# Performance work log

Hardware: AMD Instinct MI355X
Metric: run time of the kernel (lower is better)

Reference implementation:

```python
import jax, jax.numpy as jnp
import numpy as np
from jax import lax


def _conv(x, w):
    # 3x3 conv, stride 1, SAME padding, NCHW/OIHW layout, no bias
    return lax.conv_general_dilated(
        x, w, window_strides=(1, 1), padding='SAME',
        dimension_numbers=('NCHW', 'OIHW', 'NCHW'))


def _interleave2x2(tl, tr, bl, br):
    # each [B,H,W] -> [B,2H,2W] with tl at (0::2,0::2), tr at (0::2,1::2), etc.
    top = jnp.stack([tl, tr], axis=-1)          # [B,H,W,2]
    bot = jnp.stack([bl, br], axis=-1)          # [B,H,W,2]
    x = jnp.stack([top, bot], axis=2)           # [B,H,2,W,2]
    B, H, _, W, _ = x.shape
    return x.reshape(B, 2 * H, 2 * W)


def setup_inputs() -> dict:
    key = jax.random.key(0)
    ks = jax.random.split(key, 8)
    B, H, W = 16, 512, 512
    width = 12
    s = 0.1  # weight scale, approximates xavier for tiny fan-ins
    return {
        'mosaic': jax.random.normal(ks[0], (B, 4, H, W), jnp.float32),
        'fw0': jax.random.normal(ks[1], (width, 4, 3, 3), jnp.float32) * s,
        'fw1': jax.random.normal(ks[2], (width, width, 3, 3), jnp.float32) * s,
        'fw2': jax.random.normal(ks[3], (width, width, 3, 3), jnp.float32) * s,
        'ww0': jax.random.normal(ks[4], (width, 4, 3, 3), jnp.float32) * s,
        'ww1': jax.random.normal(ks[5], (width, width, 3, 3), jnp.float32) * s,
        'ww2': jax.random.normal(ks[6], (width, width, 3, 3), jnp.float32) * s,
        'cw0': jax.random.normal(ks[7], (6, 2, 3, 3), jnp.float32) * s,
    }


def reference(mosaic, fw0, fw1, fw2, ww0, ww1, ww2, cw0):
    width = fw0.shape[0]  # 12
    half = width // 2

    f = jax.nn.relu(_conv(mosaic, fw0))
    f = jax.nn.relu(_conv(f, fw1))
    interps = jax.nn.relu(_conv(f, fw2))

    w = jax.nn.relu(_conv(mosaic, ww0))
    w = jax.nn.relu(_conv(w, ww1))
    w = jax.nn.relu(_conv(w, ww2))
    weights = jax.nn.softmax(w, axis=1)

    mul = interps * weights                              # [B,12,H,W]
    # green_rb[:,0] = sum of first half, green_rb[:,1] = sum of second half
    green_rb = jnp.stack(
        [mul[:, :half].sum(axis=1), mul[:, half:].sum(axis=1)], axis=1)  # [B,2,H,W]

    # green_add channels: [mosaic0, g1, mosaic3, mosaic0, g0, mosaic3]
    green_add = jnp.stack([
        mosaic[:, 0], green_rb[:, 1], mosaic[:, 3],
        mosaic[:, 0], green_rb[:, 0], mosaic[:, 3]], axis=1)  # [B,6,H,W]

    # chroma: (rb - green_rb) -> single conv 2->6 (chroma_depth=1, no relu)
    rb = jnp.stack([mosaic[:, 1], mosaic[:, 2]], axis=1)  # [B,2,H,W]
    chroma_diff = _conv(rb - green_rb, cw0)               # [B,6,H,W]
    chroma_pred = chroma_diff + green_add

    # pixel-shuffle assembly of full-res RGB [B,3,2H,2W]
    r = _interleave2x2(chroma_pred[:, 0], mosaic[:, 1], chroma_pred[:, 1], chroma_pred[:, 2])
    g = _interleave2x2(mosaic[:, 0], green_rb[:, 0], green_rb[:, 1], mosaic[:, 3])
    b = _interleave2x2(chroma_pred[:, 3], chroma_pred[:, 4], mosaic[:, 2], chroma_pred[:, 5])
    return jnp.stack([r, g, b], axis=1)
```

## Files before the change

### kernel.cpp

```cpp
#include <hip/hip_runtime.h>
#include <cstdint>

#define HH 512
#define WW 512
#define TX 58

typedef __attribute__((ext_vector_type(8)))  short    short8;
typedef __attribute__((ext_vector_type(16))) float    f32x16;
typedef __attribute__((ext_vector_type(4)))  float    f32x4;
typedef __attribute__((ext_vector_type(2)))  unsigned u32x2;
typedef __attribute__((ext_vector_type(8)))  int      int8v;

union FragU { uint4 u; short8 s; };
union B8U   { u32x2 u2[2]; short8 s; };
union AF8   { uint4 u[2]; int8v v; };
union BF8   { unsigned d[8]; int8v v; };

#define L1F_O  0
#define L1W_O  9984
#define L1RST  832
#define MOS_O  19968
#define MOSR   512
#define L2F_O  19968
#define L2W_O  28288
#define L2RST  832
#define RELAY_O 0
#define SMEMB  36608

#define MFMA_SC(A, B, C) \
  __builtin_amdgcn_mfma_scale_f32_16x16x128_f8f6f4((A), (B), (C), 0, 0, 0, 0x7F7F7F7Fu, 0, 0x7F7F7F7Fu)

__device__ __forceinline__ unsigned cvtpk(float a, float b) {
  unsigned r;
  asm("v_cvt_pk_bf16_f32 %0, %1, %2" : "=v"(r) : "v"(a), "v"(b));
  return r;
}
__device__ __forceinline__ unsigned rpk8(float a, float b, float c, float d, bool im) {
  int r = __builtin_amdgcn_cvt_pk_fp8_f32(fmaxf(a, 0.f), fmaxf(b, 0.f), 0, false);
  r = __builtin_amdgcn_cvt_pk_fp8_f32(fmaxf(c, 0.f), fmaxf(d, 0.f), r, true);
  return im ? (unsigned)r : 0u;
}
__device__ __forceinline__ unsigned short f2bf(float f) {
  union { float f; unsigned u; } v; v.f = f;
  unsigned r = v.u + 0x7fffu + ((v.u >> 16) & 1u);
  return (unsigned short)(r >> 16);
}
__device__ __forceinline__ float bf2f(unsigned short b) {
  union { unsigned u; float f; } v; v.u = ((unsigned)b) << 16;
  return v.f;
}
__device__ __forceinline__ float lo16(unsigned u) {
  union { unsigned v; float f; } x; x.v = u << 16; return x.f;
}
__device__ __forceinline__ float hi16(unsigned u) {
  union { unsigned v; float f; } x; x.v = u & 0xffff0000u; return x.f;
}

__global__ void wt_kernel(const float* __restrict__ fw0, const float* __restrict__ fw1,
                          const float* __restrict__ fw2, const float* __restrict__ ww0,
                          const float* __restrict__ ww1, const float* __restrict__ ww2,
                          uint4* __restrict__ wsf) {
  int t = blockIdx.x * 256 + threadIdx.x;
  if (t >= 448) return;
  if (t < 192) {
    int f = t >> 6, lane = t & 63;
    int h = (lane >> 5) & 1, m = lane & 31;
    unsigned short v[8];
#pragma unroll
    for (int e = 0; e < 8; ++e) {
      int sq = 2 * h + (e >> 2);
      int c4 = e & 3;
      float w = 0.f;
      if (sq < 3 && m < 24) {
        w = (m < 12) ? fw0[(m * 4 + c4) * 9 + f * 3 + sq]
                     : ww0[((m - 12) * 4 + c4) * 9 + f * 3 + sq];
      }
      v[e] = f2bf(w);
    }
    uint4 o;
    o.x = (unsigned)v[0] | ((unsigned)v[1] << 16);
    o.y = (unsigned)v[2] | ((unsigned)v[3] << 16);
    o.z = (unsigned)v[4] | ((unsigned)v[5] << 16);
    o.w = (unsigned)v[6] | ((unsigned)v[7] << 16);
    wsf[t] = o;
  } else {
    int u = t - 192, sid = u >> 6, lane = u & 63;
    int m = lane & 15, kg = lane >> 4;
    int layer = sid >> 1, path = sid & 1;
    const float* src = layer ? (path ? ww2 : fw2) : (path ? ww1 : fw1);
    const float scale = (layer == 1 && path == 1) ? 1.44269504f : 1.0f;
    unsigned d[8];
#pragma unroll
    for (int k = 0; k < 8; ++k) {
      float w4[4];
#pragma unroll
      for (int j4 = 0; j4 < 4; ++j4) {
        int e = 4 * k + j4;
        float w = 0.f;
        if (m < 12) {
          if (kg < 3) {
            int dx = e / 12, ci = e % 12, tap = kg * 3 + dx;
            w = src[(m * 12 + ci) * 9 + tap] * scale;
          } else {
            int i = e >> 3, j = e & 7;
            if (i < 3 && j < 4) {
              int tap = i * 3 + 2, ci = 8 + j;
              w = src[(m * 12 + ci) * 9 + tap] * scale;
            }
          }
        }
        w4[j4] = w;
      }
      int x = __builtin_amdgcn_cvt_pk_fp8_f32(w4[0], w4[1], 0, false);
      x = __builtin_amdgcn_cvt_pk_fp8_f32(w4[2], w4[3], x, true);
      d[k] = (unsigned)x;
    }
    uint4* dst = wsf + 192 + sid * 128 + lane * 2;
    dst[0] = make_uint4(d[0], d[1], d[2], d[3]);
    dst[1] = make_uint4(d[4], d[5], d[6], d[7]);
  }
}

__global__ __launch_bounds__(256, 4)
void green_kernel(const float* __restrict__ mosaic, const uint4* __restrict__ wsf,
                  unsigned short* __restrict__ green) {
  __shared__ __align__(16) char s[SMEMB];
  const int tid = threadIdx.x;
  const int lane = tid & 63;
  const int wv = __builtin_amdgcn_readfirstlane(tid >> 6);
  const int h = (lane >> 5) & 1, ln = lane & 31;
  const int ln8 = ln * 8, ln12 = ln * 12;
  const int pxl = lane & 15, kg = lane >> 4;
  const int bid = blockIdx.x;
  const int bx = bid % 9;
  const int t9 = bid / 9;
  const int by = t9 & 63, b = t9 >> 6;
  const int X0 = bx * TX, Y0 = by * 8;

  {
    const float* mb = mosaic + (size_t)b * 4 * HH * WW;
    for (int p = tid; p < 14 * 64; p += 256) {
      int row = p >> 6, col = p & 63;
      int gy = Y0 + row - 3, gx = X0 + col - 3;
      float c0 = 0.f, c1 = 0.f, c2 = 0.f, c3 = 0.f;
      if ((unsigned)gy < HH && (unsigned)gx < WW) {
        const float* mp = mb + (size_t)gy * WW + gx;
        c0 = mp[0]; c1 = mp[HH * WW]; c2 = mp[2 * HH * WW]; c3 = mp[3 * HH * WW];
      }
      u32x2 w = { cvtpk(c0, c1), cvtpk(c2, c3) };
      *(u32x2*)(s + MOS_O + row * MOSR + col * 8) = w;
    }
    for (int i = tid; i < 528; i += 256) {
      int seg = i / 22, d = i - seg * 22;
      int row = seg % 12, w = seg / 12;
      *(unsigned*)(s + w * 9984 + row * 832 + 744 + d * 4) = 0u;
    }
  }
  __syncthreads();

  {
    FragU a3[3];
#pragma unroll
    for (int q = 0; q < 3; ++q) a3[q].u = wsf[q * 64 + lane];
    const char* pLo = s + MOS_O + 3 * wv * MOSR + ln8 + 16 * h;
    const char* pHi = s + MOS_O + 3 * wv * MOSR + ln8 + 8;
    char* base = s + 3 * wv * L1RST + ln12;
    char* pA = base + L1F_O + 4 * h;
    char* pB = h ? base + L1W_O : base + L1F_O + 8;
    char* pC = base + L1W_O + (h ? 8 : 4);
    bool ck[2];
    ck[0] = (unsigned)(X0 + 0  + ln - 2) < WW;
    ck[1] = (unsigned)(X0 + 30 + ln - 2) < WW;
#pragma unroll
    for (int r = 0; r < 3; ++r) {
      const int ly = 3 * wv + r;
      const bool rowok = (unsigned)(Y0 + ly - 2) < HH;
#pragma unroll
      for (int g = 0; g < 2; ++g) {
        const int cb = g * 30;
        f32x16 c = {};
#pragma unroll
        for (int ky = 0; ky < 3; ++ky) {
          B8U bu;
          bu.u2[0] = *(const u32x2*)(pLo + (r + ky) * MOSR + cb * 8);
          bu.u2[1] = *(const u32x2*)(pHi + (r + ky) * MOSR + cb * 8);
          c = __builtin_amdgcn_mfma_f32_32x32x16_bf16(a3[ky].s, bu.s, c, 0, 0, 0);
        }
        const bool im = rowok && ck[g];
        *(unsigned*)(pA + r * L1RST + cb * 12) = rpk8(c[0], c[1], c[2], c[3], im);
        *(unsigned*)(pB + r * L1RST + cb * 12) = rpk8(c[4], c[5], c[6], c[7], im);
        *(unsigned*)(pC + r * L1RST + cb * 12) = rpk8(c[8], c[9], c[10], c[11], im);
      }
    }
  }
  __syncthreads();

  {
    for (int i = tid; i < 560; i += 256) {
      int seg = i / 28, d = i - seg * 28;
      int row = seg % 10, w = seg / 10;
      *(unsigned*)(s + L2F_O + w * 8320 + row * 832 + 720 + d * 4) = 0u;
    }
    AF8 aF, aW;
    aF.u[0] = wsf[192 + lane * 2]; aF.u[1] = wsf[193 + lane * 2];
    aW.u[0] = wsf[320 + lane * 2]; aW.u[1] = wsf[321 + lane * 2];
    const int c0 = (wv == 0) ? 0 : (wv == 1) ? 16 : (wv == 2) ? 32 : 44;
    int o0, o1, o2, o3;
    if (kg < 3) { o0 = kg * L1RST + pxl * 12; o1 = o0 + 8; o2 = o0 + 16; o3 = o0 + 24; }
    else        { o0 = (pxl + 2) * 12 + 8; o1 = o0 + L1RST; o2 = o1 + L1RST; o3 = o2; }
    const char* P0 = s + L1F_O + c0 * 12 + o0;
    const char* P1 = s + L1F_O + c0 * 12 + o1;
    const char* P2 = s + L1F_O + c0 * 12 + o2;
    const char* P3 = s + L1F_O + c0 * 12 + o3;
    const bool ckx = (unsigned)(X0 + c0 + pxl - 1) < WW;
    char* pO = s + L2F_O + (c0 + pxl) * 12 + 4 * kg;
#pragma unroll
    for (int ly = 0; ly < 10; ++ly) {
      const int imm = ly * L1RST;
      BF8 bF, bW;
      bF.d[0] = *(const unsigned*)(P0 + imm);        bF.d[1] = *(const unsigned*)(P0 + imm + 4);
      bF.d[2] = *(const unsigned*)(P1 + imm);        bF.d[3] = *(const unsigned*)(P1 + imm + 4);
      bF.d[4] = *(const unsigned*)(P2 + imm);        bF.d[5] = *(const unsigned*)(P2 + imm + 4);
      bF.d[6] = *(const unsigned*)(P3 + imm);        bF.d[7] = *(const unsigned*)(P3 + imm + 4);
      bW.d[0] = *(const unsigned*)(P0 + imm + 9984); bW.d[1] = *(const unsigned*)(P0 + imm + 9988);
      bW.d[2] = *(const unsigned*)(P1 + imm + 9984); bW.d[3] = *(const unsigned*)(P1 + imm + 9988);
      bW.d[4] = *(const unsigned*)(P2 + imm + 9984); bW.d[5] = *(const unsigned*)(P2 + imm + 9988);
      bW.d[6] = *(const unsigned*)(P3 + imm + 9984); bW.d[7] = *(const unsigned*)(P3 + imm + 9988);
      f32x4 cF = {0.f, 0.f, 0.f, 0.f}, cW = {0.f, 0.f, 0.f, 0.f};
      cF = MFMA_SC(aF.v, bF.v, cF);
      cW = MFMA_SC(aW.v, bW.v, cW);
      const bool im = ckx && ((unsigned)(Y0 + ly - 1) < HH);
      if (kg < 3) {
        *(unsigned*)(pO + ly * L2RST)        = rpk8(cF[0], cF[1], cF[2], cF[3], im);
        *(unsigned*)(pO + ly * L2RST + 8320) = rpk8(cW[0], cW[1], cW[2], cW[3], im);
      }
    }
  }
  __syncthreads();

  {
    AF8 aF, aW;
    aF.u[0] = wsf[448 + lane * 2]; aF.u[1] = wsf[449 + lane * 2];
    aW.u[0] = wsf[576 + lane * 2]; aW.u[1] = wsf[577 + lane * 2];
    const int c0 = (wv == 0) ? 0 : (wv == 1) ? 16 : (wv == 2) ? 32 : 42;
    int o0, o1, o2, o3;
    if (kg < 3) { o0 = kg * L2RST + pxl * 12; o1 = o0 + 8; o2 = o0 + 16; o3 = o0 + 24; }
    else        { o0 = (pxl + 2) * 12 + 8; o1 = o0 + L2RST; o2 = o1 + L2RST; o3 = o2; }
    const char* P0 = s + L2F_O + c0 * 12 + o0;
    const char* P1 = s + L2F_O + c0 * 12 + o1;
    const char* P2 = s + L2F_O + c0 * 12 + o2;
    const char* P3 = s + L2F_O + c0 * 12 + o3;
    char* relay = s + RELAY_O + wv * 3328;
#pragma unroll
    for (int half = 0; half < 2; ++half) {
#pragma unroll
      for (int rr = 0; rr < 4; ++rr) {
        const int imm = (half * 4 + rr) * L2RST;
        BF8 bF, bW;
        bF.d[0] = *(const unsigned*)(P0 + imm);        bF.d[1] = *(const unsigned*)(P0 + imm + 4);
        bF.d[2] = *(const unsigned*)(P1 + imm);        bF.d[3] = *(const unsigned*)(P1 + imm + 4);
        bF.d[4] = *(const unsigned*)(P2 + imm);        bF.d[5] = *(const unsigned*)(P2 + imm + 4);
        bF.d[6] = *(const unsigned*)(P3 + imm);        bF.d[7] = *(const unsigned*)(P3 + imm + 4);
        bW.d[0] = *(const unsigned*)(P0 + imm + 8320); bW.d[1] = *(const unsigned*)(P0 + imm + 8324);
        bW.d[2] = *(const unsigned*)(P1 + imm + 8320); bW.d[3] = *(const unsigned*)(P1 + imm + 8324);
        bW.d[4] = *(const unsigned*)(P2 + imm + 8320); bW.d[5] = *(const unsigned*)(P2 + imm + 8324);
        bW.d[6] = *(const unsigned*)(P3 + imm + 8320); bW.d[7] = *(const unsigned*)(P3 + imm + 8324);
        f32x4 cF = {0.f, 0.f, 0.f, 0.f}, cW = {0.f, 0.f, 0.f, 0.f};
        cF = MFMA_SC(aF.v, bF.v, cF);
        cW = MFMA_SC(aW.v, bW.v, cW);
        if (kg < 3) {
          char* slot = relay + ((rr << 4) + pxl) * 52 + kg * 8;
          *(unsigned*)(slot)      = cvtpk(fmaxf(cF[0], 0.f), fmaxf(cF[1], 0.f));
          *(unsigned*)(slot + 4)  = cvtpk(fmaxf(cF[2], 0.f), fmaxf(cF[3], 0.f));
          *(unsigned*)(slot + 24) = cvtpk(fmaxf(cW[0], 0.f), fmaxf(cW[1], 0.f));
          *(unsigned*)(slot + 28) = cvtpk(fmaxf(cW[2], 0.f), fmaxf(cW[3], 0.f));
        }
      }
      asm volatile("s_waitcnt lgkmcnt(0)" ::: "memory");
      {
        const char* slot = relay + lane * 52;
        unsigned fu[6], wu[6];
#pragma unroll
        for (int i = 0; i < 6; ++i) {
          fu[i] = *(const unsigned*)(slot + i * 4);
          wu[i] = *(const unsigned*)(slot + 24 + i * 4);
        }
        float F[12], Wv[12];
#pragma unroll
        for (int i = 0; i < 6; ++i) {
          F[2 * i] = lo16(fu[i]);  F[2 * i + 1] = hi16(fu[i]);
          Wv[2 * i] = lo16(wu[i]); Wv[2 * i + 1] = hi16(wu[i]);
        }
        float m = 0.f;
#pragma unroll
        for (int c2 = 0; c2 < 12; ++c2) m = fmaxf(m, Wv[c2]);
        float sum = 0.f, s0 = 0.f, s1 = 0.f;
#pragma unroll
        for (int c2 = 0; c2 < 12; ++c2) {
          const float e = exp2f(Wv[c2] - m);
          sum += e;
          if (c2 < 6) s0 = fmaf(F[c2], e, s0);
          else        s1 = fmaf(F[c2], e, s1);
        }
        const float inv = 1.f / sum;
        const unsigned pg = cvtpk(s0 * inv, s1 * inv);
        const int gy = Y0 + half * 4 + kg;
        const int gx = X0 + c0 + pxl;
        if ((unsigned)gx < WW) {
          green[((b * 2 + 0) * HH + gy) * WW + gx] = (unsigned short)pg;
          green[((b * 2 + 1) * HH + gy) * WW + gx] = (unsigned short)(pg >> 16);
        }
      }
      asm volatile("s_waitcnt lgkmcnt(0)" ::: "memory");
    }
  }
}

__global__ __launch_bounds__(256)
void assemble_kernel(const float* __restrict__ mosaic, const unsigned short* __restrict__ green,
                     const float* __restrict__ cw0, float* __restrict__ out) {
  const int t = blockIdx.x * 256 + threadIdx.x;
  const int x = t & (WW - 1);
  const int y = (t >> 9) & (HH - 1);
  const int b = t >> 18;

  const int p = y * WW + x;
  const float* __restrict__ mb = mosaic + (size_t)b * 4 * HH * WW;
  const unsigned short* __restrict__ gb = green + (size_t)b * 2 * HH * WW;

  const float m0 = mb[p];
  const float m1 = mb[HH * WW + p];
  const float m2 = mb[2 * HH * WW + p];
  const float m3 = mb[3 * HH * WW + p];
  const float g0 = bf2f(gb[p]);
  const float g1 = bf2f(gb[HH * WW + p]);

  float cd[6] = {0.f, 0.f, 0.f, 0.f, 0.f, 0.f};
#pragma unroll
  for (int ky = 0; ky < 3; ++ky) {
#pragma unroll
    for (int kx = 0; kx < 3; ++kx) {
      const int yy = y + ky - 1, xx = x + kx - 1;
      float c0 = 0.f, c1 = 0.f;
      if ((unsigned)yy < HH && (unsigned)xx < WW) {
        const int q = yy * WW + xx;
        c0 = mb[HH * WW + q]     - bf2f(gb[q]);
        c1 = mb[2 * HH * WW + q] - bf2f(gb[HH * WW + q]);
      }
      const int k = ky * 3 + kx;
#pragma unroll
      for (int o = 0; o < 6; ++o) {
        cd[o] = fmaf(c0, cw0[(o * 2 + 0) * 9 + k], cd[o]);
        cd[o] = fmaf(c1, cw0[(o * 2 + 1) * 9 + k], cd[o]);
      }
    }
  }
  const float cp0 = cd[0] + m0;
  const float cp1 = cd[1] + g1;
  const float cp2 = cd[2] + m3;
  const float cp3 = cd[3] + m0;
  const float cp4 = cd[4] + g0;
  const float cp5 = cd[5] + m3;

  const int W2 = 2 * WW;
  const size_t plane = (size_t)(2 * HH) * W2;
  size_t base = ((size_t)(b * 3) * (2 * HH) + 2 * y) * W2 + 2 * x;
  *(float2*)(out + base)              = make_float2(cp0, m1);
  *(float2*)(out + base + W2)         = make_float2(cp1, cp2);
  *(float2*)(out + base + plane)      = make_float2(m0, g0);
  *(float2*)(out + base + plane + W2) = make_float2(g1, m3);
  *(float2*)(out + base + 2 * plane)      = make_float2(cp3, cp4);
  *(float2*)(out + base + 2 * plane + W2) = make_float2(m2, cp5);
}

extern "C" void kernel_launch(void* const* d_in, const int* in_sizes, int n_in,
                              void* d_out, int out_size, void* d_ws, size_t ws_size,
                              hipStream_t stream) {
  const float* mosaic = (const float*)d_in[0];
  const float* fw0 = (const float*)d_in[1];
  const float* fw1 = (const float*)d_in[2];
  const float* fw2 = (const float*)d_in[3];
  const float* ww0 = (const float*)d_in[4];
  const float* ww1 = (const float*)d_in[5];
  const float* ww2 = (const float*)d_in[6];
  const float* cw0 = (const float*)d_in[7];

  uint4* wsf = (uint4*)((char*)d_ws + 32768);
  unsigned short* green = (unsigned short*)((char*)d_ws + 67584);
  float* out = (float*)d_out;

  wt_kernel<<<2, 256, 0, stream>>>(fw0, fw1, fw2, ww0, ww1, ww2, wsf);
  green_kernel<<<16 * 64 * 9, 256, 0, stream>>>(mosaic, wsf, green);
  assemble_kernel<<<(16 * HH * WW) / 256, 256, 0, stream>>>(mosaic, green, cw0, out);
}
```

Before: 193.7 us.

## Fuse chroma conv and RGB assembly into green kernel via extra halo

Merges the separate assemble kernel into the green kernel. Each tile now computes green with one extra halo pixel on every side, stores it in LDS, then runs the 2->6 chroma conv and writes the interleaved RGB output directly. This removes the global write and re-read of the bf16 green planes and one kernel launch. In exchange it redoes more halo work per tile in the conv layers, uses more LDS, and lowers the occupancy bound from 4 to 3 blocks.

Measured after the change: 229.8 us. 1.19x slower.

```diff
diff --git a/kernel.cpp b/kernel.cpp
--- a/kernel.cpp
+++ b/kernel.cpp
@@ -17,15 +17,16 @@
 union BF8   { unsigned d[8]; int8v v; };
 
 #define L1F_O  0
-#define L1W_O  9984
+#define L1W_O  11648
 #define L1RST  832
-#define MOS_O  19968
-#define MOSR   512
-#define L2F_O  19968
-#define L2W_O  28288
+#define MOS_O  23296
+#define MOSR   528
+#define L2F_O  23296
+#define L2W_O  33280
 #define L2RST  832
 #define RELAY_O 0
-#define SMEMB  36608
+#define GLDS_O 13312
+#define SMEMB  43264
 
 #define MFMA_SC(A, B, C) \
   __builtin_amdgcn_mfma_scale_f32_16x16x128_f8f6f4((A), (B), (C), 0, 0, 0, 0x7F7F7F7Fu, 0, 0x7F7F7F7Fu)
@@ -44,10 +45,6 @@
   union { float f; unsigned u; } v; v.f = f;
   unsigned r = v.u + 0x7fffu + ((v.u >> 16) & 1u);
   return (unsigned short)(r >> 16);
-}
-__device__ __forceinline__ float bf2f(unsigned short b) {
-  union { unsigned u; float f; } v; v.u = ((unsigned)b) << 16;
-  return v.f;
 }
 __device__ __forceinline__ float lo16(unsigned u) {
   union { unsigned v; float f; } x; x.v = u << 16; return x.f;
@@ -121,9 +118,9 @@
   }
 }
 
-__global__ __launch_bounds__(256, 4)
+__global__ __launch_bounds__(256, 3)
 void green_kernel(const float* __restrict__ mosaic, const uint4* __restrict__ wsf,
-                  unsigned short* __restrict__ green) {
+                  const float* __restrict__ cw0, float* __restrict__ out) {
   __shared__ __align__(16) char s[SMEMB];
   const int tid = threadIdx.x;
   const int lane = tid & 63;
@@ -136,12 +133,12 @@
   const int t9 = bid / 9;
   const int by = t9 & 63, b = t9 >> 6;
   const int X0 = bx * TX, Y0 = by * 8;
+  const float* __restrict__ mb = mosaic + (size_t)b * 4 * HH * WW;
 
   {
-    const float* mb = mosaic + (size_t)b * 4 * HH * WW;
-    for (int p = tid; p < 14 * 64; p += 256) {
-      int row = p >> 6, col = p & 63;
-      int gy = Y0 + row - 3, gx = X0 + col - 3;
+    for (int p = tid; p < 16 * 66; p += 256) {
+      int row = p / 66, col = p - row * 66;
+      int gy = Y0 + row - 4, gx = X0 + col - 4;
       float c0 = 0.f, c1 = 0.f, c2 = 0.f, c3 = 0.f;
       if ((unsigned)gy < HH && (unsigned)gx < WW) {
         const float* mp = mb + (size_t)gy * WW + gx;
@@ -150,10 +147,10 @@
       u32x2 w = { cvtpk(c0, c1), cvtpk(c2, c3) };
       *(u32x2*)(s + MOS_O + row * MOSR + col * 8) = w;
     }
-    for (int i = tid; i < 528; i += 256) {
-      int seg = i / 22, d = i - seg * 22;
-      int row = seg % 12, w = seg / 12;
-      *(unsigned*)(s + w * 9984 + row * 832 + 744 + d * 4) = 0u;
+    for (int i = tid; i < 448; i += 256) {
+      int seg = i >> 4, d = i & 15;
+      int row = seg % 14, w = seg / 14;
+      *(unsigned*)(s + w * 11648 + row * 832 + 768 + d * 4) = 0u;
     }
   }
   __syncthreads();
@@ -162,49 +159,51 @@
     FragU a3[3];
 #pragma unroll
     for (int q = 0; q < 3; ++q) a3[q].u = wsf[q * 64 + lane];
-    const char* pLo = s + MOS_O + 3 * wv * MOSR + ln8 + 16 * h;
-    const char* pHi = s + MOS_O + 3 * wv * MOSR + ln8 + 8;
-    char* base = s + 3 * wv * L1RST + ln12;
+    const char* pLo = s + MOS_O + 4 * wv * MOSR + ln8 + 16 * h;
+    const char* pHi = s + MOS_O + 4 * wv * MOSR + ln8 + 8;
+    char* base = s + 4 * wv * L1RST + ln12;
     char* pA = base + L1F_O + 4 * h;
     char* pB = h ? base + L1W_O : base + L1F_O + 8;
     char* pC = base + L1W_O + (h ? 8 : 4);
     bool ck[2];
-    ck[0] = (unsigned)(X0 + 0  + ln - 2) < WW;
-    ck[1] = (unsigned)(X0 + 30 + ln - 2) < WW;
-#pragma unroll
-    for (int r = 0; r < 3; ++r) {
-      const int ly = 3 * wv + r;
-      const bool rowok = (unsigned)(Y0 + ly - 2) < HH;
-#pragma unroll
-      for (int g = 0; g < 2; ++g) {
-        const int cb = g * 30;
-        f32x16 c = {};
-#pragma unroll
-        for (int ky = 0; ky < 3; ++ky) {
-          B8U bu;
-          bu.u2[0] = *(const u32x2*)(pLo + (r + ky) * MOSR + cb * 8);
-          bu.u2[1] = *(const u32x2*)(pHi + (r + ky) * MOSR + cb * 8);
-          c = __builtin_amdgcn_mfma_f32_32x32x16_bf16(a3[ky].s, bu.s, c, 0, 0, 0);
-        }
-        const bool im = rowok && ck[g];
-        *(unsigned*)(pA + r * L1RST + cb * 12) = rpk8(c[0], c[1], c[2], c[3], im);
-        *(unsigned*)(pB + r * L1RST + cb * 12) = rpk8(c[4], c[5], c[6], c[7], im);
-        *(unsigned*)(pC + r * L1RST + cb * 12) = rpk8(c[8], c[9], c[10], c[11], im);
+    ck[0] = (unsigned)(X0 + 0  + ln - 3) < WW;
+    ck[1] = (unsigned)(X0 + 32 + ln - 3) < WW;
+#pragma unroll
+    for (int r = 0; r < 4; ++r) {
+      const int ly = 4 * wv + r;
+      if (ly < 14) {
+        const bool rowok = (unsigned)(Y0 + ly - 3) < HH;
+#pragma unroll
+        for (int g = 0; g < 2; ++g) {
+          const int cb = g * 32;
+          f32x16 c = {};
+#pragma unroll
+          for (int ky = 0; ky < 3; ++ky) {
+            B8U bu;
+            bu.u2[0] = *(const u32x2*)(pLo + (r + ky) * MOSR + cb * 8);
+            bu.u2[1] = *(const u32x2*)(pHi + (r + ky) * MOSR + cb * 8);
+            c = __builtin_amdgcn_mfma_f32_32x32x16_bf16(a3[ky].s, bu.s, c, 0, 0, 0);
+          }
+          const bool im = rowok && ck[g];
+          *(unsigned*)(pA + r * L1RST + cb * 12) = rpk8(c[0], c[1], c[2], c[3], im);
+          *(unsigned*)(pB + r * L1RST + cb * 12) = rpk8(c[4], c[5], c[6], c[7], im);
+          *(unsigned*)(pC + r * L1RST + cb * 12) = rpk8(c[8], c[9], c[10], c[11], im);
+        }
       }
     }
   }
   __syncthreads();
 
   {
-    for (int i = tid; i < 560; i += 256) {
-      int seg = i / 28, d = i - seg * 28;
-      int row = seg % 10, w = seg / 10;
-      *(unsigned*)(s + L2F_O + w * 8320 + row * 832 + 720 + d * 4) = 0u;
+    for (int i = tid; i < 528; i += 256) {
+      int seg = i / 22, d = i - seg * 22;
+      int row = seg % 12, w = seg / 12;
+      *(unsigned*)(s + L2F_O + w * 9984 + row * 832 + 744 + d * 4) = 0u;
     }
     AF8 aF, aW;
     aF.u[0] = wsf[192 + lane * 2]; aF.u[1] = wsf[193 + lane * 2];
     aW.u[0] = wsf[320 + lane * 2]; aW.u[1] = wsf[321 + lane * 2];
-    const int c0 = (wv == 0) ? 0 : (wv == 1) ? 16 : (wv == 2) ? 32 : 44;
+    const int c0 = (wv == 0) ? 0 : (wv == 1) ? 16 : (wv == 2) ? 32 : 46;
     int o0, o1, o2, o3;
     if (kg < 3) { o0 = kg * L1RST + pxl * 12; o1 = o0 + 8; o2 = o0 + 16; o3 = o0 + 24; }
     else        { o0 = (pxl + 2) * 12 + 8; o1 = o0 + L1RST; o2 = o1 + L1RST; o3 = o2; }
@@ -212,27 +211,27 @@
     const char* P1 = s + L1F_O + c0 * 12 + o1;
     const char* P2 = s + L1F_O + c0 * 12 + o2;
     const char* P3 = s + L1F_O + c0 * 12 + o3;
-    const bool ckx = (unsigned)(X0 + c0 + pxl - 1) < WW;
+    const bool ckx = (unsigned)(X0 + c0 + pxl - 2) < WW;
     char* pO = s + L2F_O + (c0 + pxl) * 12 + 4 * kg;
 #pragma unroll
-    for (int ly = 0; ly < 10; ++ly) {
+    for (int ly = 0; ly < 12; ++ly) {
       const int imm = ly * L1RST;
       BF8 bF, bW;
-      bF.d[0] = *(const unsigned*)(P0 + imm);        bF.d[1] = *(const unsigned*)(P0 + imm + 4);
-      bF.d[2] = *(const unsigned*)(P1 + imm);        bF.d[3] = *(const unsigned*)(P1 + imm + 4);
-      bF.d[4] = *(const unsigned*)(P2 + imm);        bF.d[5] = *(const unsigned*)(P2 + imm + 4);
-      bF.d[6] = *(const unsigned*)(P3 + imm);        bF.d[7] = *(const unsigned*)(P3 + imm + 4);
-      bW.d[0] = *(const unsigned*)(P0 + imm + 9984); bW.d[1] = *(const unsigned*)(P0 + imm + 9988);
-      bW.d[2] = *(const unsigned*)(P1 + imm + 9984); bW.d[3] = *(const unsigned*)(P1 + imm + 9988);
-      bW.d[4] = *(const unsigned*)(P2 + imm + 9984); bW.d[5] = *(const unsigned*)(P2 + imm + 9988);
-      bW.d[6] = *(const unsigned*)(P3 + imm + 9984); bW.d[7] = *(const unsigned*)(P3 + imm + 9988);
+      bF.d[0] = *(const unsigned*)(P0 + imm);         bF.d[1] = *(const unsigned*)(P0 + imm + 4);
+      bF.d[2] = *(const unsigned*)(P1 + imm);         bF.d[3] = *(const unsigned*)(P1 + imm + 4);
+      bF.d[4] = *(const unsigned*)(P2 + imm);         bF.d[5] = *(const unsigned*)(P2 + imm + 4);
+      bF.d[6] = *(const unsigned*)(P3 + imm);         bF.d[7] = *(const unsigned*)(P3 + imm + 4);
+      bW.d[0] = *(const unsigned*)(P0 + imm + 11648); bW.d[1] = *(const unsigned*)(P0 + imm + 11652);
+      bW.d[2] = *(const unsigned*)(P1 + imm + 11648); bW.d[3] = *(const unsigned*)(P1 + imm + 11652);
+      bW.d[4] = *(const unsigned*)(P2 + imm + 11648); bW.d[5] = *(const unsigned*)(P2 + imm + 11652);
+      bW.d[6] = *(const unsigned*)(P3 + imm + 11648); bW.d[7] = *(const unsigned*)(P3 + imm + 11652);
       f32x4 cF = {0.f, 0.f, 0.f, 0.f}, cW = {0.f, 0.f, 0.f, 0.f};
       cF = MFMA_SC(aF.v, bF.v, cF);
       cW = MFMA_SC(aW.v, bW.v, cW);
-      const bool im = ckx && ((unsigned)(Y0 + ly - 1) < HH);
+      const bool im = ckx && ((unsigned)(Y0 + ly - 2) < HH);
       if (kg < 3) {
         *(unsigned*)(pO + ly * L2RST)        = rpk8(cF[0], cF[1], cF[2], cF[3], im);
-        *(unsigned*)(pO + ly * L2RST + 8320) = rpk8(cW[0], cW[1], cW[2], cW[3], im);
+        *(unsigned*)(pO + ly * L2RST + 9984) = rpk8(cW[0], cW[1], cW[2], cW[3], im);
       }
     }
   }
@@ -242,7 +241,7 @@
     AF8 aF, aW;
     aF.u[0] = wsf[448 + lane * 2]; aF.u[1] = wsf[449 + lane * 2];
     aW.u[0] = wsf[576 + lane * 2]; aW.u[1] = wsf[577 + lane * 2];
-    const int c0 = (wv == 0) ? 0 : (wv == 1) ? 16 : (wv == 2) ? 32 : 42;
+    const int c0 = (wv == 0) ? 0 : (wv == 1) ? 16 : (wv == 2) ? 32 : 44;
     int o0, o1, o2, o3;
     if (kg < 3) { o0 = kg * L2RST + pxl * 12; o1 = o0 + 8; o2 = o0 + 16; o3 = o0 + 24; }
     else        { o0 = (pxl + 2) * 12 + 8; o1 = o0 + L2RST; o2 = o1 + L2RST; o3 = o2; }
@@ -252,125 +251,119 @@
     const char* P3 = s + L2F_O + c0 * 12 + o3;
     char* relay = s + RELAY_O + wv * 3328;
 #pragma unroll
-    for (int half = 0; half < 2; ++half) {
+    for (int r2 = 0; r2 < 3; ++r2) {
 #pragma unroll
       for (int rr = 0; rr < 4; ++rr) {
-        const int imm = (half * 4 + rr) * L2RST;
-        BF8 bF, bW;
-        bF.d[0] = *(const unsigned*)(P0 + imm);        bF.d[1] = *(const unsigned*)(P0 + imm + 4);
-        bF.d[2] = *(const unsigned*)(P1 + imm);        bF.d[3] = *(const unsigned*)(P1 + imm + 4);
-        bF.d[4] = *(const unsigned*)(P2 + imm);        bF.d[5] = *(const unsigned*)(P2 + imm + 4);
-        bF.d[6] = *(const unsigned*)(P3 + imm);        bF.d[7] = *(const unsigned*)(P3 + imm + 4);
-        bW.d[0] = *(const unsigned*)(P0 + imm + 8320); bW.d[1] = *(const unsigned*)(P0 + imm + 8324);
-        bW.d[2] = *(const unsigned*)(P1 + imm + 8320); bW.d[3] = *(const unsigned*)(P1 + imm + 8324);
-        bW.d[4] = *(const unsigned*)(P2 + imm + 8320); bW.d[5] = *(const unsigned*)(P2 + imm + 8324);
-        bW.d[6] = *(const unsigned*)(P3 + imm + 8320); bW.d[7] = *(const unsigned*)(P3 + imm + 8324);
-        f32x4 cF = {0.f, 0.f, 0.f, 0.f}, cW = {0.f, 0.f, 0.f, 0.f};
-        cF = MFMA_SC(aF.v, bF.v, cF);
-        cW = MFMA_SC(aW.v, bW.v, cW);
-        if (kg < 3) {
-          char* slot = relay + ((rr << 4) + pxl) * 52 + kg * 8;
-          *(unsigned*)(slot)      = cvtpk(fmaxf(cF[0], 0.f), fmaxf(cF[1], 0.f));
-          *(unsigned*)(slot + 4)  = cvtpk(fmaxf(cF[2], 0.f), fmaxf(cF[3], 0.f));
-          *(unsigned*)(slot + 24) = cvtpk(fmaxf(cW[0], 0.f), fmaxf(cW[1], 0.f));
-          *(unsigned*)(slot + 28) = cvtpk(fmaxf(cW[2], 0.f), fmaxf(cW[3], 0.f));
+        const int ly = r2 * 4 + rr;
+        if (ly < 10) {
+          const int imm = ly * L2RST;
+          BF8 bF, bW;
+          bF.d[0] = *(const unsigned*)(P0 + imm);        bF.d[1] = *(const unsigned*)(P0 + imm + 4);
+          bF.d[2] = *(const unsigned*)(P1 + imm);        bF.d[3] = *(const unsigned*)(P1 + imm + 4);
+          bF.d[4] = *(const unsigned*)(P2 + imm);        bF.d[5] = *(const unsigned*)(P2 + imm + 4);
+          bF.d[6] = *(const unsigned*)(P3 + imm);        bF.d[7] = *(const unsigned*)(P3 + imm + 4);
+          bW.d[0] = *(const unsigned*)(P0 + imm + 9984); bW.d[1] = *(const unsigned*)(P0 + imm + 9988);
+          bW.d[2] = *(const unsigned*)(P1 + imm + 9984); bW.d[3] = *(const unsigned*)(P1 + imm + 9988);
+          bW.d[4] = *(const unsigned*)(P2 + imm + 9984); bW.d[5] = *(const unsigned*)(P2 + imm + 9988);
+          bW.d[6] = *(const unsigned*)(P3 + imm + 9984); bW.d[7] = *(const unsigned*)(P3 + imm + 9988);
+          f32x4 cF = {0.f, 0.f, 0.f, 0.f}, cW = {0.f, 0.f, 0.f, 0.f};
+          cF = MFMA_SC(aF.v, bF.v, cF);
+          cW = MFMA_SC(aW.v, bW.v, cW);
+          if (kg < 3) {
+            char* slot = relay + ((rr << 4) + pxl) * 52 + kg * 8;
+            *(unsigned*)(slot)      = cvtpk(fmaxf(cF[0], 0.f), fmaxf(cF[1], 0.f));
+            *(unsigned*)(slot + 4)  = cvtpk(fmaxf(cF[2], 0.f), fmaxf(cF[3], 0.f));
+            *(unsigned*)(slot + 24) = cvtpk(fmaxf(cW[0], 0.f), fmaxf(cW[1], 0.f));
+            *(unsigned*)(slot + 28) = cvtpk(fmaxf(cW[2], 0.f), fmaxf(cW[3], 0.f));
+          }
         }
       }
       asm volatile("s_waitcnt lgkmcnt(0)" ::: "memory");
       {
-        const char* slot = relay + lane * 52;
-        unsigned fu[6], wu[6];
-#pragma unroll
-        for (int i = 0; i < 6; ++i) {
-          fu[i] = *(const unsigned*)(slot + i * 4);
-          wu[i] = *(const unsigned*)(slot + 24 + i * 4);
-        }
-        float F[12], Wv[12];
-#pragma unroll
-        for (int i = 0; i < 6; ++i) {
-          F[2 * i] = lo16(fu[i]);  F[2 * i + 1] = hi16(fu[i]);
-          Wv[2 * i] = lo16(wu[i]); Wv[2 * i + 1] = hi16(wu[i]);
-        }
-        float m = 0.f;
-#pragma unroll
-        for (int c2 = 0; c2 < 12; ++c2) m = fmaxf(m, Wv[c2]);
-        float sum = 0.f, s0 = 0.f, s1 = 0.f;
-#pragma unroll
-        for (int c2 = 0; c2 < 12; ++c2) {
-          const float e = exp2f(Wv[c2] - m);
-          sum += e;
-          if (c2 < 6) s0 = fmaf(F[c2], e, s0);
-          else        s1 = fmaf(F[c2], e, s1);
-        }
-        const float inv = 1.f / sum;
-        const unsigned pg = cvtpk(s0 * inv, s1 * inv);
-        const int gy = Y0 + half * 4 + kg;
-        const int gx = X0 + c0 + pxl;
-        if ((unsigned)gx < WW) {
-          green[((b * 2 + 0) * HH + gy) * WW + gx] = (unsigned short)pg;
-          green[((b * 2 + 1) * HH + gy) * WW + gx] = (unsigned short)(pg >> 16);
+        const int row = r2 * 4 + kg;
+        if (row < 10) {
+          const char* slot = relay + lane * 52;
+          unsigned fu[6], wu[6];
+#pragma unroll
+          for (int i = 0; i < 6; ++i) {
+            fu[i] = *(const unsigned*)(slot + i * 4);
+            wu[i] = *(const unsigned*)(slot + 24 + i * 4);
+          }
+          float F[12], Wv[12];
+#pragma unroll
+          for (int i = 0; i < 6; ++i) {
+            F[2 * i] = lo16(fu[i]);  F[2 * i + 1] = hi16(fu[i]);
+            Wv[2 * i] = lo16(wu[i]); Wv[2 * i + 1] = hi16(wu[i]);
+          }
+          float m = 0.f;
+#pragma unroll
+          for (int c2 = 0; c2 < 12; ++c2) m = fmaxf(m, Wv[c2]);
+          float sum = 0.f, s0 = 0.f, s1 = 0.f;
+#pragma unroll
+          for (int c2 = 0; c2 < 12; ++c2) {
+            const float e = exp2f(Wv[c2] - m);
+            sum += e;
+            if (c2 < 6) s0 = fmaf(F[c2], e, s0);
+            else        s1 = fmaf(F[c2], e, s1);
+          }
+          const float inv = 1.f / sum;
+          *(unsigned*)(s + GLDS_O + (row * 60 + c0 + pxl) * 4) = cvtpk(s0 * inv, s1 * inv);
         }
       }
       asm volatile("s_waitcnt lgkmcnt(0)" ::: "memory");
     }
   }
-}
-
-__global__ __launch_bounds__(256)
-void assemble_kernel(const float* __restrict__ mosaic, const unsigned short* __restrict__ green,
-                     const float* __restrict__ cw0, float* __restrict__ out) {
-  const int t = blockIdx.x * 256 + threadIdx.x;
-  const int x = t & (WW - 1);
-  const int y = (t >> 9) & (HH - 1);
-  const int b = t >> 18;
-
-  const int p = y * WW + x;
-  const float* __restrict__ mb = mosaic + (size_t)b * 4 * HH * WW;
-  const unsigned short* __restrict__ gb = green + (size_t)b * 2 * HH * WW;
-
-  const float m0 = mb[p];
-  const float m1 = mb[HH * WW + p];
-  const float m2 = mb[2 * HH * WW + p];
-  const float m3 = mb[3 * HH * WW + p];
-  const float g0 = bf2f(gb[p]);
-  const float g1 = bf2f(gb[HH * WW + p]);
-
-  float cd[6] = {0.f, 0.f, 0.f, 0.f, 0.f, 0.f};
-#pragma unroll
-  for (int ky = 0; ky < 3; ++ky) {
-#pragma unroll
-    for (int kx = 0; kx < 3; ++kx) {
-      const int yy = y + ky - 1, xx = x + kx - 1;
-      float c0 = 0.f, c1 = 0.f;
-      if ((unsigned)yy < HH && (unsigned)xx < WW) {
-        const int q = yy * WW + xx;
-        c0 = mb[HH * WW + q]     - bf2f(gb[q]);
-        c1 = mb[2 * HH * WW + q] - bf2f(gb[HH * WW + q]);
-      }
-      const int k = ky * 3 + kx;
-#pragma unroll
-      for (int o = 0; o < 6; ++o) {
-        cd[o] = fmaf(c0, cw0[(o * 2 + 0) * 9 + k], cd[o]);
-        cd[o] = fmaf(c1, cw0[(o * 2 + 1) * 9 + k], cd[o]);
-      }
-    }
-  }
-  const float cp0 = cd[0] + m0;
-  const float cp1 = cd[1] + g1;
-  const float cp2 = cd[2] + m3;
-  const float cp3 = cd[3] + m0;
-  const float cp4 = cd[4] + g0;
-  const float cp5 = cd[5] + m3;
-
-  const int W2 = 2 * WW;
-  const size_t plane = (size_t)(2 * HH) * W2;
-  size_t base = ((size_t)(b * 3) * (2 * HH) + 2 * y) * W2 + 2 * x;
-  *(float2*)(out + base)              = make_float2(cp0, m1);
-  *(float2*)(out + base + W2)         = make_float2(cp1, cp2);
-  *(float2*)(out + base + plane)      = make_float2(m0, g0);
-  *(float2*)(out + base + plane + W2) = make_float2(g1, m3);
-  *(float2*)(out + base + 2 * plane)      = make_float2(cp3, cp4);
-  *(float2*)(out + base + 2 * plane + W2) = make_float2(m2, cp5);
+  __syncthreads();
+
+  for (int i = tid; i < 8 * TX; i += 256) {
+    const int orow = i / TX, ocol = i - orow * TX;
+    const int gy = Y0 + orow, gx = X0 + ocol;
+    const int p = gy * WW + gx;
+    const unsigned gpk = *(const unsigned*)(s + GLDS_O + ((orow + 1) * 60 + ocol + 1) * 4);
+    const float g0 = lo16(gpk), g1 = hi16(gpk);
+    float cd[6] = {0.f, 0.f, 0.f, 0.f, 0.f, 0.f};
+#pragma unroll
+    for (int ky = 0; ky < 3; ++ky) {
+#pragma unroll
+      for (int kx = 0; kx < 3; ++kx) {
+        const int yy = gy + ky - 1, xx = gx + kx - 1;
+        float c0 = 0.f, c1 = 0.f;
+        if ((unsigned)yy < HH && (unsigned)xx < WW) {
+          const int q = yy * WW + xx;
+          const unsigned gg = *(const unsigned*)(s + GLDS_O + ((orow + ky) * 60 + ocol + kx) * 4);
+          c0 = mb[HH * WW + q]     - lo16(gg);
+          c1 = mb[2 * HH * WW + q] - hi16(gg);
+        }
+        const int k = ky * 3 + kx;
+#pragma unroll
+        for (int o = 0; o < 6; ++o) {
+          cd[o] = fmaf(c0, cw0[(o * 2 + 0) * 9 + k], cd[o]);
+          cd[o] = fmaf(c1, cw0[(o * 2 + 1) * 9 + k], cd[o]);
+        }
+      }
+    }
+    if (gx < WW) {
+      const float m0 = mb[p];
+      const float m1 = mb[HH * WW + p];
+      const float m2 = mb[2 * HH * WW + p];
+      const float m3 = mb[3 * HH * WW + p];
+      const float cp0 = cd[0] + m0;
+      const float cp1 = cd[1] + g1;
+      const float cp2 = cd[2] + m3;
+      const float cp3 = cd[3] + m0;
+      const float cp4 = cd[4] + g0;
+      const float cp5 = cd[5] + m3;
+      const int W2 = 2 * WW;
+      const size_t plane = (size_t)(2 * HH) * W2;
+      size_t base = ((size_t)(b * 3) * (2 * HH) + 2 * gy) * W2 + 2 * gx;
+      *(float2*)(out + base)              = make_float2(cp0, m1);
+      *(float2*)(out + base + W2)         = make_float2(cp1, cp2);
+      *(float2*)(out + base + plane)      = make_float2(m0, g0);
+      *(float2*)(out + base + plane + W2) = make_float2(g1, m3);
+      *(float2*)(out + base + 2 * plane)      = make_float2(cp3, cp4);
+      *(float2*)(out + base + 2 * plane + W2) = make_float2(m2, cp5);
+    }
+  }
 }
 
 extern "C" void kernel_launch(void* const* d_in, const int* in_sizes, int n_in,
@@ -386,10 +379,8 @@
   const float* cw0 = (const float*)d_in[7];
 
   uint4* wsf = (uint4*)((char*)d_ws + 32768);
-  unsigned short* green = (unsigned short*)((char*)d_ws + 67584);
   float* out = (float*)d_out;
 
   wt_kernel<<<2, 256, 0, stream>>>(fw0, fw1, fw2, ww0, ww1, ww2, wsf);
-  green_kernel<<<16 * 64 * 9, 256, 0, stream>>>(mosaic, wsf, green);
-  assemble_kernel<<<(16 * HH * WW) / 256, 256, 0, stream>>>(mosaic, green, cw0, out);
-}
+  green_kernel<<<16 * 64 * 9, 256, 0, stream>>>(mosaic, wsf, cw0, out);
+}
```
